# Optimization experiments

Hardware: AMD Instinct MI355X
Metric: run time of the kernel (lower is better)

Reference implementation:

```python
import jax, jax.numpy as jnp
import numpy as np

H = 512  # hidden_size


def setup_inputs() -> dict:
    key = jax.random.key(0)
    ks = jax.random.split(key, 8)
    B, L_tgt, L_src = 4, 32, 1024
    query = jax.random.normal(ks[0], (B, L_tgt, H), dtype=jnp.float32)
    states = jax.random.normal(ks[1], (B, L_src, 2 * H), dtype=jnp.float32)
    source_mask = jnp.ones((B, L_src), dtype=jnp.int32)
    s = 0.02
    Wq = jax.random.normal(ks[2], (H, 2 * H), dtype=jnp.float32) * s      # _linear_query.weight^T
    bq = jax.random.normal(ks[3], (2 * H,), dtype=jnp.float32) * s        # _linear_query.bias
    Ws = jax.random.normal(ks[4], (2 * H, 2 * H), dtype=jnp.float32) * s  # _linear_source.weight^T (no bias)
    v = jax.random.normal(ks[5], (2 * H,), dtype=jnp.float32) * s         # _v.weight (no bias)
    Wc = jax.random.normal(ks[6], (3 * H, H), dtype=jnp.float32) * s      # _context.weight^T
    bc = jax.random.normal(ks[7], (H,), dtype=jnp.float32) * s            # _context.bias
    return {"query": query, "states": states, "source_mask": source_mask,
            "Wq": Wq, "bq": bq, "Ws": Ws, "v": v, "Wc": Wc, "bc": bc}


def reference(query, states, source_mask, Wq, bq, Ws, v, Wc, bc):
    # Bahdanau additive attention.
    # query: (B, T, H), states: (B, S, 2H), source_mask: (B, S)
    qf = query @ Wq + bq                         # (B, T, 2H)
    sf = states @ Ws                             # (B, S, 2H)
    # alignments: v . tanh(qf[:, :, None] + sf[:, None, :])  -> (B, T, S)
    feats = jnp.tanh(qf[:, :, None, :] + sf[:, None, :, :])  # (B, T, S, 2H)
    alignments = jnp.einsum('btsd,d->bts', feats, v)
    # mask (B, S) -> (B, 1, S); masked positions get -inf before softmax
    alignments = jnp.where(source_mask[:, None, :].astype(bool), alignments, -jnp.inf)
    attentions = jax.nn.softmax(alignments, axis=2)           # (B, T, S)
    context = jnp.einsum('bts,bsd->btd', attentions, states)  # (B, T, 2H)
    concat_context = jnp.concatenate((context, query), axis=2)  # (B, T, 3H)
    attention_hidden = concat_context @ Wc + bc               # (B, T, H)
    attentions_t = jnp.swapaxes(attentions, 1, 2)             # (B, S, T)
    return (context, attention_hidden, attentions_t)
```

## Files before the change

### kernel.cpp

```cpp
#include <hip/hip_runtime.h>
#include <math.h>


typedef unsigned short u16;
typedef __bf16 bf16x8 __attribute__((ext_vector_type(8)));
typedef float floatx4 __attribute__((ext_vector_type(4)));

#define B_ 4
#define T_ 32
#define S_ 1024
#define H_ 512
#define D_ 1024
#define BT_ 128
#define TWO_LOG2E 2.8853900817779268f
#define LOG2E 1.4426950408889634f

__device__ __forceinline__ float bf2f(u16 u) {
  unsigned int i = ((unsigned int)u) << 16;
  return __builtin_bit_cast(float, i);
}
__device__ __forceinline__ u16 f2bf(float f) {
  unsigned int i = __builtin_bit_cast(unsigned int, f);
  i += 0x7fffu + ((i >> 16) & 1u);
  return (u16)(i >> 16);
}
__device__ __forceinline__ void ld_g2l_16(const u16* g, u16* l) {
  __builtin_amdgcn_global_load_lds((__attribute__((address_space(1))) void*)(u16*)g,
                                   (__attribute__((address_space(3))) void*)l, 16, 0, 0);
}


__global__ __launch_bounds__(256) void prep_fused5(const float* __restrict__ states, const float* __restrict__ Ws,
                                                   const float* __restrict__ query, const float* __restrict__ Wq,
                                                   const float* __restrict__ bq,
                                                   const float* __restrict__ Wc, const float* __restrict__ bc,
                                                   u16* __restrict__ sbf, u16* __restrict__ sbfT,
                                                   u16* __restrict__ WsT, float* __restrict__ qfp,
                                                   float* __restrict__ rowsum, float* __restrict__ hid) {
  __shared__ u16 tile[32][65];
  __shared__ float q[8][128];
  const int t = threadIdx.x;
  if (blockIdx.x < 512) {
    if (blockIdx.x == 0 && t < 128) rowsum[t] = 0.f;
    const int n0 = (blockIdx.x & 15) * 64, k0 = (blockIdx.x >> 4) * 32;
    const int kr = t >> 3, nc = (t & 7) * 8;
    const float* p = Ws + (size_t)(k0 + kr) * D_ + n0 + nc;
    float4 a = *(const float4*)p, b = *(const float4*)(p + 4);
    tile[kr][nc + 0] = f2bf(a.x); tile[kr][nc + 1] = f2bf(a.y);
    tile[kr][nc + 2] = f2bf(a.z); tile[kr][nc + 3] = f2bf(a.w);
    tile[kr][nc + 4] = f2bf(b.x); tile[kr][nc + 5] = f2bf(b.y);
    tile[kr][nc + 6] = f2bf(b.z); tile[kr][nc + 7] = f2bf(b.w);
    __syncthreads();
    const int nr = t >> 2, kc = (t & 3) * 8;
    union { uint4 v; u16 s[8]; } st;
#pragma unroll
    for (int i = 0; i < 8; ++i) st.s[i] = tile[kc + i][nr];
    *(uint4*)(WsT + (size_t)(n0 + nr) * D_ + k0 + kc) = st.v;
  } else if (blockIdx.x < 2560) {
    const int bid = blockIdx.x - 512;
    const int b = bid >> 9;
    const int r2 = bid & 511;
    const int d0 = (r2 & 15) * 64, s0 = (r2 >> 4) * 32;
    const int sr = t >> 3, dc = (t & 7) * 8;
    const float* p = states + ((size_t)b * S_ + s0 + sr) * D_ + d0 + dc;
    float4 a = *(const float4*)p, bb = *(const float4*)(p + 4);
    union { uint4 v; u16 s[8]; } pk;
    pk.s[0] = f2bf(a.x); pk.s[1] = f2bf(a.y); pk.s[2] = f2bf(a.z); pk.s[3] = f2bf(a.w);
    pk.s[4] = f2bf(bb.x); pk.s[5] = f2bf(bb.y); pk.s[6] = f2bf(bb.z); pk.s[7] = f2bf(bb.w);
    *(uint4*)(sbf + ((size_t)b * S_ + s0 + sr) * D_ + d0 + dc) = pk.v;
#pragma unroll
    for (int i = 0; i < 8; ++i) tile[sr][dc + i] = pk.s[i];
    __syncthreads();
    const int dr = t >> 2, sc = (t & 3) * 8;
    union { uint4 v; u16 s[8]; } st;
#pragma unroll
    for (int i = 0; i < 8; ++i) st.s[i] = tile[sc + i][dr];
    *(uint4*)(sbfT + ((size_t)b * D_ + d0 + dr) * S_ + s0 + sc) = st.v;
  } else if (blockIdx.x < 2816) {
    const int idx = blockIdx.x - 2560;
    const int c0 = (idx & 3) * 256, r0 = ((idx >> 2) & 15) * 8, ks = idx >> 6;
    const int k0 = ks * 128;
    for (int i = t; i < 8 * 128; i += 256) {
      const int rl = i >> 7, kk = i & 127;
      q[rl][kk] = query[(size_t)(r0 + rl) * H_ + k0 + kk];
    }
    __syncthreads();
    const int col = c0 + t;
    float acc[8] = {};
    for (int kk = 0; kk < 128; ++kk) {
      const float w = Wq[(size_t)(k0 + kk) * D_ + col];
#pragma unroll
      for (int r = 0; r < 8; ++r) acc[r] = fmaf(q[r][kk], w, acc[r]);
    }
    const float bb = (ks == 0) ? bq[col] : 0.f;
    float* dst = qfp + (size_t)ks * (BT_ * D_);
#pragma unroll
    for (int r = 0; r < 8; ++r)
      dst[(size_t)(r0 + r) * D_ + col] = TWO_LOG2E * (acc[r] + bb);
  } else {
    const int idx = blockIdx.x - 2816;
    const int c0 = (idx & 1) * 256, r0 = ((idx >> 1) & 15) * 8, ks = idx >> 5;
    const int k0 = ks * 128;
    for (int i = t; i < 8 * 128; i += 256) {
      const int rl = i >> 7, kk = i & 127;
      q[rl][kk] = query[(size_t)(r0 + rl) * H_ + k0 + kk];
    }
    __syncthreads();
    const int col = c0 + t;
    float acc[8] = {};
    for (int kk = 0; kk < 128; ++kk) {
      const float w = Wc[(size_t)(D_ + k0 + kk) * H_ + col];
#pragma unroll
      for (int r = 0; r < 8; ++r) acc[r] = fmaf(q[r][kk], w, acc[r]);
    }
    const float bb = (ks == 0) ? bc[col] : 0.f;
#pragma unroll
    for (int r = 0; r < 8; ++r)
      atomicAdd(&hid[(size_t)(r0 + r) * H_ + col], acc[r] + bb);
  }
}

__device__ __forceinline__ void f2f_stage(const u16* __restrict__ A, const u16* __restrict__ BT,
                                          u16* sAb, u16* sBb, int bm0, int bn0, int k0,
                                          int wv, int srow, int sp) {
#pragma unroll
  for (int j = 0; j < 4; ++j) {
    const int r = wv * 32 + j * 8 + srow;
    const int c = sp ^ (r & 7);
    ld_g2l_16(A + (size_t)(bm0 + r) * D_ + k0 + c * 8, sAb + (wv * 32 + j * 8) * 64);
  }
#pragma unroll
  for (int j = 0; j < 2; ++j) {
    const int r = wv * 16 + j * 8 + srow;
    const int c = sp ^ (r & 7);
    ld_g2l_16(BT + (size_t)(bn0 + r) * D_ + k0 + c * 8, sBb + (wv * 16 + j * 8) * 64);
  }
}

__device__ __forceinline__ void f2f_compute(const u16* sAb, const u16* sBb,
                                            int wm, int wn, int fm, int fq, floatx4 (&acc)[4][2]) {
#pragma unroll
  for (int win = 0; win < 2; ++win) {
    bf16x8 af[4], bfr[2];
#pragma unroll
    for (int i = 0; i < 4; ++i) {
      const int R = wm + i * 16 + fm;
      af[i] = *(const bf16x8*)&sAb[R * 64 + ((win * 4 + fq) ^ (R & 7)) * 8];
    }
#pragma unroll
    for (int j = 0; j < 2; ++j) {
      const int R = wn + j * 16 + fm;
      bfr[j] = *(const bf16x8*)&sBb[R * 64 + ((win * 4 + fq) ^ (R & 7)) * 8];
    }
#pragma unroll
    for (int i = 0; i < 4; ++i)
#pragma unroll
      for (int j = 0; j < 2; ++j)
        acc[i][j] = __builtin_amdgcn_mfma_f32_16x16x32_bf16(af[i], bfr[j], acc[i][j], 0, 0, 0);
  }
}

__global__ __launch_bounds__(256) void f2i_sfgemm(const u16* __restrict__ A, const u16* __restrict__ BT,
                                                  const float* __restrict__ qfp, float* __restrict__ Eq,
                                                  u16* __restrict__ Es) {
  __shared__ __align__(16) u16 sA[2][128 * 64];
  __shared__ __align__(16) u16 sB[2][64 * 64];
  const int bm0 = blockIdx.y * 128, bn0 = blockIdx.x * 64;
  const int t = threadIdx.x;
  const int wv = t >> 6, lane = t & 63;
  const int wm = (wv >> 1) * 64, wn = (wv & 1) * 32;
  const int fm = lane & 15, fq = lane >> 4;
  const int srow = lane >> 3, sp = lane & 7;

  {
    const int bid = blockIdx.y * 16 + blockIdx.x;
    const int idx = bid * 256 + t;
    const float s = qfp[idx] + qfp[BT_ * D_ + idx] +
                    qfp[2 * BT_ * D_ + idx] + qfp[3 * BT_ * D_ + idx];
    Eq[idx] = __builtin_amdgcn_exp2f(s);
  }

  floatx4 acc[4][2];
  const floatx4 fz = {0.f, 0.f, 0.f, 0.f};
#pragma unroll
  for (int i = 0; i < 4; ++i) { acc[i][0] = fz; acc[i][1] = fz; }

  f2f_stage(A, BT, sA[0], sB[0], bm0, bn0, 0, wv, srow, sp);
#pragma unroll 1
  for (int k0 = 0; k0 < D_; k0 += 128) {
    f2f_stage(A, BT, sA[1], sB[1], bm0, bn0, k0 + 64, wv, srow, sp);
    asm volatile("s_waitcnt vmcnt(6)" ::: "memory");
    __builtin_amdgcn_s_barrier();
    f2f_compute(sA[0], sB[0], wm, wn, fm, fq, acc);
    __builtin_amdgcn_s_barrier();
    if (k0 + 128 < D_) {
      f2f_stage(A, BT, sA[0], sB[0], bm0, bn0, k0 + 128, wv, srow, sp);
      asm volatile("s_waitcnt vmcnt(6)" ::: "memory");
    } else {
      asm volatile("s_waitcnt vmcnt(0)" ::: "memory");
    }
    __builtin_amdgcn_s_barrier();
    f2f_compute(sA[1], sB[1], wm, wn, fm, fq, acc);
    __builtin_amdgcn_s_barrier();
  }
#pragma unroll
  for (int i = 0; i < 4; ++i)
#pragma unroll
    for (int j = 0; j < 2; ++j)
#pragma unroll
      for (int r = 0; r < 4; ++r) {
        const int row = bm0 + wm + i * 16 + fq * 4 + r;
        const int col = bn0 + wn + j * 16 + fm;
        Es[(size_t)row * D_ + col] = f2bf(__builtin_amdgcn_exp2f(TWO_LOG2E * acc[i][j][r]));
      }
}

__global__ __launch_bounds__(256) void f3j_align(const float* __restrict__ Eq, const u16* __restrict__ Es,
                                                 const float* __restrict__ v, const int* __restrict__ mask,
                                                 u16* __restrict__ pbf, float* __restrict__ rowsum) {
  __shared__ float red[32][4];
  const int w = (blockIdx.x * 256 + threadIdx.x) >> 6;
  const int lane = threadIdx.x & 63;
  const int wv = threadIdx.x >> 6;
  const int b = w >> 9;
  const int s0 = (w & 511) * 2;
  const int msk0 = mask[(size_t)b * S_ + s0];
  const int msk1 = mask[(size_t)b * S_ + s0 + 1];
  float vm2[16], es0[16], es1[16];
  float sumv = 0.f;
  {
    union { uint4 u[2]; u16 h[16]; } ua, ub;
    const uint4* ep0 = (const uint4*)(Es + ((size_t)b * S_ + s0) * D_ + lane * 16);
    const uint4* ep1 = (const uint4*)(Es + ((size_t)b * S_ + s0 + 1) * D_ + lane * 16);
    ua.u[0] = ep0[0]; ua.u[1] = ep0[1];
    ub.u[0] = ep1[0]; ub.u[1] = ep1[1];
    const float4* vp = (const float4*)(v + lane * 16);
#pragma unroll
    for (int c = 0; c < 4; ++c) {
      const float4 w4 = vp[c];
      vm2[4 * c + 0] = -2.f * w4.x; vm2[4 * c + 1] = -2.f * w4.y;
      vm2[4 * c + 2] = -2.f * w4.z; vm2[4 * c + 3] = -2.f * w4.w;
      sumv += w4.x + w4.y + w4.z + w4.w;
    }
#pragma unroll
    for (int j = 0; j < 16; ++j) { es0[j] = bf2f(ua.h[j]); es1[j] = bf2f(ub.h[j]); }
  }
  const float* qbase = Eq + ((size_t)(b * T_)) * D_ + lane * 16;
  for (int tc = 0; tc < 8; ++tc) {
    float sa[4], sb[4];
#pragma unroll
    for (int ti = 0; ti < 4; ++ti) {
      const float4* qp = (const float4*)(qbase + (size_t)(tc * 4 + ti) * D_);
      float a0 = sumv, a1 = sumv;
#pragma unroll
      for (int c = 0; c < 4; ++c) {
        const float4 q4 = qp[c];
        const float xs[4] = {q4.x, q4.y, q4.z, q4.w};
#pragma unroll
        for (int u2 = 0; u2 < 4; ++u2) {
          const int j = 4 * c + u2;
          a0 = fmaf(vm2[j], __builtin_amdgcn_rcpf(fmaf(xs[u2], es0[j], 1.f)), a0);
          a1 = fmaf(vm2[j], __builtin_amdgcn_rcpf(fmaf(xs[u2], es1[j], 1.f)), a1);
        }
      }
      sa[ti] = a0; sb[ti] = a1;
    }
#pragma unroll
    for (int off = 32; off > 0; off >>= 1)
#pragma unroll
      for (int ti = 0; ti < 4; ++ti) {
        sa[ti] += __shfl_xor(sa[ti], off);
        sb[ti] += __shfl_xor(sb[ti], off);
      }
    if (lane == 0) {
#pragma unroll
      for (int ti = 0; ti < 4; ++ti) {
        const int tt = tc * 4 + ti;
        const float e0 = msk0 ? __builtin_amdgcn_exp2f(sa[ti] * LOG2E) : 0.f;
        const float e1 = msk1 ? __builtin_amdgcn_exp2f(sb[ti] * LOG2E) : 0.f;
        const u16 p0 = f2bf(e0), p1 = f2bf(e1);
        *(unsigned int*)&pbf[((size_t)(b * T_ + tt)) * S_ + s0] =
            (unsigned int)p0 | ((unsigned int)p1 << 16);
        red[tt][wv] = bf2f(p0) + bf2f(p1);
      }
    }
  }
  __syncthreads();
  if (threadIdx.x < 32) {
    const int bb = blockIdx.x >> 7;
    const float rs = red[threadIdx.x][0] + red[threadIdx.x][1] +
                     red[threadIdx.x][2] + red[threadIdx.x][3];
    atomicAdd(&rowsum[bb * 32 + threadIdx.x], rs);
  }
}

__global__ __launch_bounds__(256) void f5d_context(const u16* __restrict__ pbf, const u16* __restrict__ sbfT,
                                                   const float* __restrict__ rowsum,
                                                   float* __restrict__ ctx, float* __restrict__ out_at) {
  __shared__ float rinv[32];
  const int b = blockIdx.x >> 4, dt = blockIdx.x & 15;
  if (threadIdx.x < 32) rinv[threadIdx.x] = 1.f / rowsum[b * 32 + threadIdx.x];
  __syncthreads();
  const int wv = threadIdx.x >> 6, lane = threadIdx.x & 63;
  const int n0 = dt * 64 + wv * 16;
  const int fm = lane & 15, fq = lane >> 4;
  const floatx4 fz = {0.f, 0.f, 0.f, 0.f};
  floatx4 acc0 = fz, acc1 = fz;
  const u16* pa0 = pbf + ((size_t)b * T_ + fm) * S_ + fq * 8;
  const u16* pa1 = pbf + ((size_t)b * T_ + 16 + fm) * S_ + fq * 8;
  const u16* pb  = sbfT + ((size_t)b * D_ + n0 + fm) * S_ + fq * 8;
#pragma unroll 4
  for (int k0 = 0; k0 < S_; k0 += 32) {
    bf16x8 a0 = *(const bf16x8*)(pa0 + k0);
    bf16x8 a1 = *(const bf16x8*)(pa1 + k0);
    bf16x8 bb = *(const bf16x8*)(pb + k0);
    acc0 = __builtin_amdgcn_mfma_f32_16x16x32_bf16(a0, bb, acc0, 0, 0, 0);
    acc1 = __builtin_amdgcn_mfma_f32_16x16x32_bf16(a1, bb, acc1, 0, 0, 0);
  }
  const int col = n0 + fm;
#pragma unroll
  for (int r = 0; r < 4; ++r) {
    const int t0r = fq * 4 + r;
    ctx[((size_t)b * T_ + t0r) * D_ + col] = acc0[r] * rinv[t0r];
    ctx[((size_t)b * T_ + 16 + t0r) * D_ + col] = acc1[r] * rinv[16 + t0r];
  }
  const int s0 = dt * 64;
  for (int i = threadIdx.x; i < 64 * 32; i += 256) {
    const int tt = i >> 6, sl = i & 63;
    const float e = bf2f(pbf[((size_t)(b * T_ + tt)) * S_ + s0 + sl]);
    out_at[((size_t)(b * S_ + s0 + sl)) * T_ + tt] = e * rinv[tt];
  }
}

__global__ __launch_bounds__(256) void f6c_outproj(const float* __restrict__ ctx,
                                                   const float* __restrict__ Wc,
                                                   float* __restrict__ out_hid) {
  __shared__ float cq[16][128];
  const int c0 = blockIdx.x * 128, r0 = blockIdx.y * 16, k0 = blockIdx.z * 128;
  const int tid = threadIdx.x;
  const int cl = tid & 127, rh = tid >> 7;
  for (int i = tid; i < 16 * 128; i += 256) {
    const int rl = i >> 7, kk = i & 127;
    cq[rl][kk] = ctx[(size_t)(r0 + rl) * D_ + k0 + kk];
  }
  __syncthreads();
  float acc[8] = {};
  for (int kk = 0; kk < 128; ++kk) {
    const float w = Wc[(size_t)(k0 + kk) * H_ + c0 + cl];
#pragma unroll
    for (int rr = 0; rr < 8; ++rr) acc[rr] = fmaf(cq[rh * 8 + rr][kk], w, acc[rr]);
  }
#pragma unroll
  for (int rr = 0; rr < 8; ++rr)
    atomicAdd(&out_hid[(size_t)(r0 + rh * 8 + rr) * H_ + c0 + cl], acc[rr]);
}


__global__ __launch_bounds__(256) void prep_fused(const float* __restrict__ states, const float* __restrict__ Ws,
                                                  const float* __restrict__ query, const float* __restrict__ Wq,
                                                  const float* __restrict__ bq,
                                                  u16* __restrict__ sbf, u16* __restrict__ sbfT,
                                                  u16* __restrict__ WsT, float* __restrict__ qf) {
  __shared__ u16 tile[32][65];
  __shared__ float q[8][128];
  const int t = threadIdx.x;
  if (blockIdx.x < 512) {
    const int n0 = (blockIdx.x & 15) * 64, k0 = (blockIdx.x >> 4) * 32;
    const int kr = t >> 3, nc = (t & 7) * 8;
    const float* p = Ws + (size_t)(k0 + kr) * D_ + n0 + nc;
    float4 a = *(const float4*)p, b = *(const float4*)(p + 4);
    tile[kr][nc + 0] = f2bf(a.x); tile[kr][nc + 1] = f2bf(a.y);
    tile[kr][nc + 2] = f2bf(a.z); tile[kr][nc + 3] = f2bf(a.w);
    tile[kr][nc + 4] = f2bf(b.x); tile[kr][nc + 5] = f2bf(b.y);
    tile[kr][nc + 6] = f2bf(b.z); tile[kr][nc + 7] = f2bf(b.w);
    __syncthreads();
    const int nr = t >> 2, kc = (t & 3) * 8;
    union { uint4 v; u16 s[8]; } st;
#pragma unroll
    for (int i = 0; i < 8; ++i) st.s[i] = tile[kc + i][nr];
    *(uint4*)(WsT + (size_t)(n0 + nr) * D_ + k0 + kc) = st.v;
  } else if (blockIdx.x < 2560) {
    const int bid = blockIdx.x - 512;
    const int b = bid >> 9;
    const int r2 = bid & 511;
    const int d0 = (r2 & 15) * 64, s0 = (r2 >> 4) * 32;
    const int sr = t >> 3, dc = (t & 7) * 8;
    const float* p = states + ((size_t)b * S_ + s0 + sr) * D_ + d0 + dc;
    float4 a = *(const float4*)p, bb = *(const float4*)(p + 4);
    union { uint4 v; u16 s[8]; } pk;
    pk.s[0] = f2bf(a.x); pk.s[1] = f2bf(a.y); pk.s[2] = f2bf(a.z); pk.s[3] = f2bf(a.w);
    pk.s[4] = f2bf(bb.x); pk.s[5] = f2bf(bb.y); pk.s[6] = f2bf(bb.z); pk.s[7] = f2bf(bb.w);
    *(uint4*)(sbf + ((size_t)b * S_ + s0 + sr) * D_ + d0 + dc) = pk.v;
#pragma unroll
    for (int i = 0; i < 8; ++i) tile[sr][dc + i] = pk.s[i];
    __syncthreads();
    const int dr = t >> 2, sc = (t & 3) * 8;
    union { uint4 v; u16 s[8]; } st;
#pragma unroll
    for (int i = 0; i < 8; ++i) st.s[i] = tile[sc + i][dr];
    *(uint4*)(sbfT + ((size_t)b * D_ + d0 + dr) * S_ + s0 + sc) = st.v;
  } else {
    const int idx = blockIdx.x - 2560;
    const int c0 = (idx & 3) * 256, r0 = ((idx >> 2) & 15) * 8, k0 = (idx >> 6) * 128;
    for (int i = t; i < 8 * 128; i += 256) {
      const int rl = i >> 7, kk = i & 127;
      q[rl][kk] = query[(size_t)(r0 + rl) * H_ + k0 + kk];
    }
    __syncthreads();
    const int col = c0 + t;
    float acc[8] = {};
    for (int kk = 0; kk < 128; ++kk) {
      const float w = Wq[(size_t)(k0 + kk) * D_ + col];
#pragma unroll
      for (int r = 0; r < 8; ++r) acc[r] = fmaf(q[r][kk], w, acc[r]);
    }
    const float bb = (k0 == 0) ? bq[col] : 0.f;
#pragma unroll
    for (int r = 0; r < 8; ++r)
      atomicAdd(&qf[(size_t)(r0 + r) * D_ + col], TWO_LOG2E * (acc[r] + bb));
  }
}

__global__ __launch_bounds__(256) void f2e_sfgemm(const u16* __restrict__ A, const u16* __restrict__ BT,
                                                  u16* __restrict__ Cb) {
  __shared__ __align__(16) u16 sA[128 * 64];
  __shared__ __align__(16) u16 sB[64 * 64];
  const int bm0 = blockIdx.y * 128, bn0 = blockIdx.x * 64;
  const int t = threadIdx.x;
  const int wv = t >> 6, lane = t & 63;
  const int wm = (wv >> 1) * 64, wn = (wv & 1) * 32;
  const int fm = lane & 15, fq = lane >> 4;
  const int srow = lane >> 3, sp = lane & 7;

  floatx4 acc[4][2];
  const floatx4 fz = {0.f, 0.f, 0.f, 0.f};
#pragma unroll
  for (int i = 0; i < 4; ++i) { acc[i][0] = fz; acc[i][1] = fz; }

  for (int k0 = 0; k0 < D_; k0 += 64) {
    __syncthreads();
#pragma unroll
    for (int j = 0; j < 4; ++j) {
      const int r = wv * 32 + j * 8 + srow;
      const int c = sp ^ (r & 7);
      ld_g2l_16(A + (size_t)(bm0 + r) * D_ + k0 + c * 8, &sA[(wv * 32 + j * 8) * 64]);
    }
#pragma unroll
    for (int j = 0; j < 2; ++j) {
      const int r = wv * 16 + j * 8 + srow;
      const int c = sp ^ (r & 7);
      ld_g2l_16(BT + (size_t)(bn0 + r) * D_ + k0 + c * 8, &sB[(wv * 16 + j * 8) * 64]);
    }
    __syncthreads();
#pragma unroll
    for (int win = 0; win < 2; ++win) {
      bf16x8 af[4], bfr[2];
#pragma unroll
      for (int i = 0; i < 4; ++i) {
        const int R = wm + i * 16 + fm;
        af[i] = *(const bf16x8*)&sA[R * 64 + ((win * 4 + fq) ^ (R & 7)) * 8];
      }
#pragma unroll
      for (int j = 0; j < 2; ++j) {
        const int R = wn + j * 16 + fm;
        bfr[j] = *(const bf16x8*)&sB[R * 64 + ((win * 4 + fq) ^ (R & 7)) * 8];
      }
#pragma unroll
      for (int i = 0; i < 4; ++i)
#pragma unroll
        for (int j = 0; j < 2; ++j)
          acc[i][j] = __builtin_amdgcn_mfma_f32_16x16x32_bf16(af[i], bfr[j], acc[i][j], 0, 0, 0);
    }
  }
#pragma unroll
  for (int i = 0; i < 4; ++i)
#pragma unroll
    for (int j = 0; j < 2; ++j)
#pragma unroll
      for (int r = 0; r < 4; ++r) {
        const int row = bm0 + wm + i * 16 + fq * 4 + r;
        const int col = bn0 + wn + j * 16 + fm;
        Cb[(size_t)row * D_ + col] = f2bf(TWO_LOG2E * acc[i][j][r]);
      }
}

__global__ __launch_bounds__(256, 6) void f3f_align(const float* __restrict__ qf, const u16* __restrict__ sfb,
                                                    const float* __restrict__ v, float* __restrict__ alg) {
  const int wid = (blockIdx.x * 256 + threadIdx.x) >> 6;
  const int lane = threadIdx.x & 63;
  const int b = wid >> 10, s = wid & 1023;
  const int t0 = blockIdx.y * 16;
  float vr[16], sr[16];
  {
    union { uint4 v[2]; u16 s[16]; } u;
    const uint4* sp = (const uint4*)(sfb + (size_t)wid * D_ + lane * 16);
    u.v[0] = sp[0]; u.v[1] = sp[1];
    const float* vp = v + lane * 16;
#pragma unroll
    for (int c = 0; c < 4; ++c) {
      float4 w = *(const float4*)(vp + 4 * c);
      vr[4 * c + 0] = w.x; vr[4 * c + 1] = w.y; vr[4 * c + 2] = w.z; vr[4 * c + 3] = w.w;
    }
#pragma unroll
    for (int j = 0; j < 16; ++j) sr[j] = bf2f(u.s[j]);
  }
  float sum[16];
#pragma unroll
  for (int tt = 0; tt < 16; ++tt) sum[tt] = 0.f;

  const float* qbase = qf + ((size_t)(b * T_ + t0)) * D_ + lane * 16;
  for (int tt = 0; tt < 16; ++tt) {
    const float4* qp = (const float4*)(qbase + (size_t)tt * D_);
    float acc = 0.f;
#pragma unroll
    for (int c = 0; c < 4; ++c) {
      float4 q4 = qp[c];
      float xs[4] = {q4.x, q4.y, q4.z, q4.w};
#pragma unroll
      for (int u2 = 0; u2 < 4; ++u2) {
        const int j = 4 * c + u2;
        const float x = xs[u2] + sr[j];
        const float e = __builtin_amdgcn_exp2f(x);
        acc = fmaf(vr[j], fmaf(-2.f, __builtin_amdgcn_rcpf(e + 1.f), 1.f), acc);
      }
    }
    sum[tt] = acc;
  }
#pragma unroll
  for (int off = 32; off > 0; off >>= 1)
#pragma unroll
    for (int tt = 0; tt < 16; ++tt) sum[tt] += __shfl_xor(sum[tt], off);
  if (lane == 0) {
#pragma unroll
    for (int tt = 0; tt < 16; ++tt)
      alg[((size_t)(b * T_ + t0 + tt)) * S_ + s] = sum[tt];
  }
}

__global__ __launch_bounds__(256) void f4b_softmax(const float* __restrict__ alg, const int* __restrict__ mask,
                                                   float* __restrict__ out_at, u16* __restrict__ pbf) {
  const int r = blockIdx.x;
  const int b = r >> 5, t = r & 31;
  const int tid = threadIdx.x;
  __shared__ float red[256];
  float a[4];
#pragma unroll
  for (int jj = 0; jj < 4; ++jj) {
    const int s = tid + 256 * jj;
    const float x = alg[(size_t)r * S_ + s];
    a[jj] = (mask[(size_t)b * S_ + s] != 0) ? x : -3.0e38f;
  }
  float m = fmaxf(fmaxf(a[0], a[1]), fmaxf(a[2], a[3]));
  red[tid] = m; __syncthreads();
  for (int st = 128; st > 0; st >>= 1) { if (tid < st) red[tid] = fmaxf(red[tid], red[tid + st]); __syncthreads(); }
  m = red[0]; __syncthreads();
  float e[4], lsum = 0.f;
#pragma unroll
  for (int jj = 0; jj < 4; ++jj) {
    e[jj] = (a[jj] > -1.0e38f) ? expf(a[jj] - m) : 0.f;
    lsum += e[jj];
  }
  red[tid] = lsum; __syncthreads();
  for (int st = 128; st > 0; st >>= 1) { if (tid < st) red[tid] += red[tid + st]; __syncthreads(); }
  const float rs = 1.f / red[0];
#pragma unroll
  for (int jj = 0; jj < 4; ++jj) {
    const int s = tid + 256 * jj;
    const float p = e[jj] * rs;
    out_at[((size_t)b * S_ + s) * T_ + t] = p;
    pbf[(size_t)r * S_ + s] = f2bf(p);
  }
}

__global__ __launch_bounds__(256) void f5c_context(const u16* __restrict__ pbf, const u16* __restrict__ sbfT,
                                                   float* __restrict__ ctx) {
  const int b = blockIdx.x >> 4, dt = blockIdx.x & 15;
  const int wv = threadIdx.x >> 6, lane = threadIdx.x & 63;
  const int n0 = dt * 64 + wv * 16;
  const int fm = lane & 15, fq = lane >> 4;
  const floatx4 fz = {0.f, 0.f, 0.f, 0.f};
  floatx4 acc0 = fz, acc1 = fz;
  const u16* pa0 = pbf + ((size_t)b * T_ + fm) * S_ + fq * 8;
  const u16* pa1 = pbf + ((size_t)b * T_ + 16 + fm) * S_ + fq * 8;
  const u16* pb  = sbfT + ((size_t)b * D_ + n0 + fm) * S_ + fq * 8;
#pragma unroll 4
  for (int k0 = 0; k0 < S_; k0 += 32) {
    bf16x8 a0 = *(const bf16x8*)(pa0 + k0);
    bf16x8 a1 = *(const bf16x8*)(pa1 + k0);
    bf16x8 bb = *(const bf16x8*)(pb + k0);
    acc0 = __builtin_amdgcn_mfma_f32_16x16x32_bf16(a0, bb, acc0, 0, 0, 0);
    acc1 = __builtin_amdgcn_mfma_f32_16x16x32_bf16(a1, bb, acc1, 0, 0, 0);
  }
  const int col = n0 + fm;
#pragma unroll
  for (int r = 0; r < 4; ++r) {
    ctx[((size_t)b * T_ + fq * 4 + r) * D_ + col] = acc0[r];
    ctx[((size_t)b * T_ + 16 + fq * 4 + r) * D_ + col] = acc1[r];
  }
}

__global__ __launch_bounds__(256) void f6b_outproj(const float* __restrict__ ctx, const float* __restrict__ query,
                                                   const float* __restrict__ Wc, const float* __restrict__ bc,
                                                   float* __restrict__ out_hid) {
  __shared__ float cq[16][128];
  const int c0 = blockIdx.x * 128, r0 = blockIdx.y * 16, k0 = blockIdx.z * 128;
  const int tid = threadIdx.x;
  const int cl = tid & 127, rh = tid >> 7;
  for (int i = tid; i < 16 * 128; i += 256) {
    const int rl = i >> 7, kk = i & 127;
    const int k = k0 + kk, row = r0 + rl;
    cq[rl][kk] = (k < D_) ? ctx[(size_t)row * D_ + k] : query[(size_t)row * H_ + k - D_];
  }
  __syncthreads();
  float acc[8] = {};
  for (int kk = 0; kk < 128; ++kk) {
    const float w = Wc[(size_t)(k0 + kk) * H_ + c0 + cl];
#pragma unroll
    for (int rr = 0; rr < 8; ++rr) acc[rr] = fmaf(cq[rh * 8 + rr][kk], w, acc[rr]);
  }
  const float bb = (blockIdx.z == 0) ? bc[c0 + cl] : 0.f;
#pragma unroll
  for (int rr = 0; rr < 8; ++rr)
    atomicAdd(&out_hid[(size_t)(r0 + rh * 8 + rr) * H_ + c0 + cl], acc[rr] + bb);
}


__global__ __launch_bounds__(256) void kc_cvt(const float* __restrict__ in, u16* __restrict__ out) {
  const size_t i0 = ((size_t)blockIdx.x * 256 + threadIdx.x) * 8;
  float4 a = *(const float4*)(in + i0);
  float4 b = *(const float4*)(in + i0 + 4);
  union { uint4 v; u16 s[8]; } r;
  r.s[0] = f2bf(a.x); r.s[1] = f2bf(a.y); r.s[2] = f2bf(a.z); r.s[3] = f2bf(a.w);
  r.s[4] = f2bf(b.x); r.s[5] = f2bf(b.y); r.s[6] = f2bf(b.z); r.s[7] = f2bf(b.w);
// ... 128 lines not shown
    *(uint4*)&sA[arow * 40 + akc + 8] = pa.v[1];
    *(uint4*)&sB[brow * 40 + bkc] = vb;
    __syncthreads();
    bf16x8 af[4], bfr[2];
#pragma unroll
    for (int i = 0; i < 4; ++i) af[i] = *(const bf16x8*)&sA[(wm + i * 16 + fm) * 40 + fq * 8];
#pragma unroll
    for (int j = 0; j < 2; ++j) bfr[j] = *(const bf16x8*)&sB[(wn + j * 16 + fm) * 40 + fq * 8];
#pragma unroll
    for (int i = 0; i < 4; ++i)
#pragma unroll
      for (int j = 0; j < 2; ++j)
        acc[i][j] = __builtin_amdgcn_mfma_f32_16x16x32_bf16(af[i], bfr[j], acc[i][j], 0, 0, 0);
  }
#pragma unroll
  for (int i = 0; i < 4; ++i)
#pragma unroll
    for (int j = 0; j < 2; ++j)
#pragma unroll
      for (int r = 0; r < 4; ++r) {
        const int row = bm0 + wm + i * 16 + fq * 4 + r;
        const int col = bn0 + wn + j * 16 + fm;
        Cb[(size_t)row * D_ + col] = f2bf(TWO_LOG2E * acc[i][j][r]);
      }
}

__global__ __launch_bounds__(256) void f4_softmax(const float* __restrict__ alg, const int* __restrict__ mask,
                                                  float* __restrict__ attn) {
  const int r = blockIdx.x;
  const int b = r >> 5;
  const int tid = threadIdx.x;
  __shared__ float red[256];
  float a[4];
#pragma unroll
  for (int jj = 0; jj < 4; ++jj) {
    const int s = tid + 256 * jj;
    const float x = alg[(size_t)r * S_ + s];
    a[jj] = (mask[(size_t)b * S_ + s] != 0) ? x : -3.0e38f;
  }
  float m = fmaxf(fmaxf(a[0], a[1]), fmaxf(a[2], a[3]));
  red[tid] = m; __syncthreads();
  for (int st = 128; st > 0; st >>= 1) { if (tid < st) red[tid] = fmaxf(red[tid], red[tid + st]); __syncthreads(); }
  m = red[0]; __syncthreads();
  float e[4], lsum = 0.f;
#pragma unroll
  for (int jj = 0; jj < 4; ++jj) {
    e[jj] = (a[jj] > -1.0e38f) ? expf(a[jj] - m) : 0.f;
    lsum += e[jj];
  }
  red[tid] = lsum; __syncthreads();
  for (int st = 128; st > 0; st >>= 1) { if (tid < st) red[tid] += red[tid + st]; __syncthreads(); }
  const float rs = 1.f / red[0];
#pragma unroll
  for (int jj = 0; jj < 4; ++jj)
    attn[(size_t)r * S_ + tid + 256 * jj] = e[jj] * rs;
}

__global__ __launch_bounds__(256) void f5b_context(const float* __restrict__ attn, const u16* __restrict__ sbf,
                                                   float* __restrict__ ctx, float* __restrict__ out_at) {
  __shared__ float at[16][64];
  const int s0 = blockIdx.x * 64, t0 = blockIdx.y * 16, b = blockIdx.z;
  const int tid = threadIdx.x;
  for (int i = tid; i < 16 * 64; i += 256) {
    const int tl = i >> 6, sl = i & 63;
    at[tl][sl] = attn[(size_t)(b * T_ + t0 + tl) * S_ + s0 + sl];
  }
  __syncthreads();
  for (int i = tid; i < 64 * 16; i += 256) {
    const int sl = i >> 4, tl = i & 15;
    out_at[((size_t)b * S_ + s0 + sl) * T_ + t0 + tl] = at[tl][sl];
  }
  float acc[16][4] = {};
  for (int sl = 0; sl < 64; ++sl) {
    const u16* srow = sbf + ((size_t)b * S_ + s0 + sl) * D_ + tid;
    float sv[4];
#pragma unroll
    for (int jj = 0; jj < 4; ++jj) sv[jj] = bf2f(srow[256 * jj]);
#pragma unroll
    for (int tl = 0; tl < 16; ++tl) {
      const float w = at[tl][sl];
#pragma unroll
      for (int jj = 0; jj < 4; ++jj) acc[tl][jj] = fmaf(w, sv[jj], acc[tl][jj]);
    }
  }
#pragma unroll
  for (int tl = 0; tl < 16; ++tl)
#pragma unroll
    for (int jj = 0; jj < 4; ++jj)
      atomicAdd(&ctx[(size_t)(b * T_ + t0 + tl) * D_ + tid + 256 * jj], acc[tl][jj]);
}

__global__ __launch_bounds__(256) void f5_context(const float* __restrict__ attn, const float* __restrict__ states,
                                                  float* __restrict__ ctx, float* __restrict__ out_at) {
  __shared__ float at[16][64];
  const int s0 = blockIdx.x * 64, t0 = blockIdx.y * 16, b = blockIdx.z;
  const int tid = threadIdx.x;
  for (int i = tid; i < 16 * 64; i += 256) {
    const int tl = i >> 6, sl = i & 63;
    at[tl][sl] = attn[(size_t)(b * T_ + t0 + tl) * S_ + s0 + sl];
  }
  __syncthreads();
  for (int i = tid; i < 64 * 16; i += 256) {
    const int sl = i >> 4, tl = i & 15;
    out_at[((size_t)b * S_ + s0 + sl) * T_ + t0 + tl] = at[tl][sl];
  }
  float acc[16][4] = {};
  for (int sl = 0; sl < 64; ++sl) {
    const float* srow = states + ((size_t)b * S_ + s0 + sl) * D_ + tid;
    float sv[4];
#pragma unroll
    for (int jj = 0; jj < 4; ++jj) sv[jj] = srow[256 * jj];
#pragma unroll
    for (int tl = 0; tl < 16; ++tl) {
      const float w = at[tl][sl];
#pragma unroll
      for (int jj = 0; jj < 4; ++jj) acc[tl][jj] = fmaf(w, sv[jj], acc[tl][jj]);
    }
  }
#pragma unroll
  for (int tl = 0; tl < 16; ++tl)
#pragma unroll
    for (int jj = 0; jj < 4; ++jj)
      atomicAdd(&ctx[(size_t)(b * T_ + t0 + tl) * D_ + tid + 256 * jj], acc[tl][jj]);
}


__global__ __launch_bounds__(256) void k1_qf(const float* __restrict__ query, const float* __restrict__ Wq,
                                             const float* __restrict__ bq, float* __restrict__ qf) {
  const int r = blockIdx.x;
  const int tid = threadIdx.x;
  __shared__ float q[H_];
  for (int i = tid; i < H_; i += 256) q[i] = query[(size_t)r * H_ + i];
  __syncthreads();
#pragma unroll
  for (int jj = 0; jj < 4; ++jj) {
    const int j = tid + 256 * jj;
    float acc = bq[j];
    for (int k = 0; k < H_; ++k) acc = fmaf(q[k], Wq[(size_t)k * D_ + j], acc);
    qf[(size_t)r * D_ + j] = acc;
  }
}

__global__ __launch_bounds__(256) void k23_align(const float* __restrict__ states, const float* __restrict__ Ws,
                                                 const float* __restrict__ v, const float* __restrict__ qf,
                                                 float* __restrict__ alg) {
  const int b = blockIdx.x >> 6;
  const int s0 = (blockIdx.x & 63) * 16;
  const int tid = threadIdx.x, lane = tid & 63, wv = tid >> 6;
  __shared__ u16 stL[16 * D_];
  __shared__ float vvL[D_];
  __shared__ float red[16 * 4];
  for (int i = tid; i < 16 * D_; i += 256) {
    const int row = i >> 10, col = i & (D_ - 1);
    stL[i] = f2bf(states[((size_t)b * S_ + s0 + row) * D_ + col]);
  }
  for (int i = tid; i < D_; i += 256) vvL[i] = v[i];
  __syncthreads();
  float acc[64];
#pragma unroll
  for (int i = 0; i < 64; ++i) acc[i] = 0.f;
#pragma unroll 4
  for (int k = 0; k < D_; ++k) {
    float wsv[4];
#pragma unroll
    for (int jj = 0; jj < 4; ++jj) wsv[jj] = Ws[(size_t)k * D_ + tid + 256 * jj];
#pragma unroll
    for (int i = 0; i < 16; ++i) {
      const float sv = bf2f(stL[i * D_ + k]);
#pragma unroll
      for (int jj = 0; jj < 4; ++jj) acc[i * 4 + jj] = fmaf(sv, wsv[jj], acc[i * 4 + jj]);
    }
  }
  for (int t = 0; t < T_; ++t) {
    float qv[4];
#pragma unroll
    for (int jj = 0; jj < 4; ++jj) qv[jj] = qf[((size_t)b * T_ + t) * D_ + tid + 256 * jj];
    float part[16];
#pragma unroll
    for (int i = 0; i < 16; ++i) {
      float p = 0.f;
#pragma unroll
      for (int jj = 0; jj < 4; ++jj)
        p = fmaf(vvL[tid + 256 * jj], tanhf(qv[jj] + acc[i * 4 + jj]), p);
      part[i] = p;
    }
#pragma unroll
    for (int i = 0; i < 16; ++i) {
      float x = part[i];
#pragma unroll
      for (int off = 32; off > 0; off >>= 1) x += __shfl_xor(x, off);
      if (lane == 0) red[i * 4 + wv] = x;
    }
    __syncthreads();
    if (tid < 16)
      alg[((size_t)b * T_ + t) * S_ + s0 + tid] =
          red[tid * 4 + 0] + red[tid * 4 + 1] + red[tid * 4 + 2] + red[tid * 4 + 3];
    __syncthreads();
  }
}

__global__ __launch_bounds__(256) void k4_softmax(const float* __restrict__ alg, const int* __restrict__ mask,
                                                  float* __restrict__ attn) {
  const int r = blockIdx.x;
  const int b = r >> 5;
  const int tid = threadIdx.x;
  __shared__ float red[256];
  float a[4];
#pragma unroll
  for (int jj = 0; jj < 4; ++jj) {
    const int s = tid + 256 * jj;
    const float x = alg[(size_t)r * S_ + s];
    a[jj] = (mask[(size_t)b * S_ + s] != 0) ? x : -3.0e38f;
  }
  float m = fmaxf(fmaxf(a[0], a[1]), fmaxf(a[2], a[3]));
  red[tid] = m; __syncthreads();
  for (int st = 128; st > 0; st >>= 1) { if (tid < st) red[tid] = fmaxf(red[tid], red[tid + st]); __syncthreads(); }
  m = red[0]; __syncthreads();
  float e[4], lsum = 0.f;
#pragma unroll
  for (int jj = 0; jj < 4; ++jj) {
    e[jj] = (a[jj] > -1.0e38f) ? expf(a[jj] - m) : 0.f;
    lsum += e[jj];
  }
  red[tid] = lsum; __syncthreads();
  for (int st = 128; st > 0; st >>= 1) { if (tid < st) red[tid] += red[tid + st]; __syncthreads(); }
  const float rs = 1.f / red[0];
#pragma unroll
  for (int jj = 0; jj < 4; ++jj)
    attn[(size_t)r * S_ + tid + 256 * jj] = e[jj] * rs;
}

__global__ __launch_bounds__(256) void k56_ctx_proj(const float* __restrict__ attn, const float* __restrict__ states,
                                                    const float* __restrict__ query, const float* __restrict__ Wc,
                                                    const float* __restrict__ bc,
                                                    float* __restrict__ out_ctx, float* __restrict__ out_hid,
                                                    float* __restrict__ out_at) {
  const int r = blockIdx.x;
  const int b = r >> 5, t = r & (T_ - 1);
  const int tid = threadIdx.x;
  __shared__ float pr[S_];
  __shared__ float cq[D_ + H_];
  for (int s = tid; s < S_; s += 256) pr[s] = attn[(size_t)r * S_ + s];
  __syncthreads();
  for (int s = tid; s < S_; s += 256) out_at[((size_t)b * S_ + s) * T_ + t] = pr[s];
  float acc[4] = {0.f, 0.f, 0.f, 0.f};
  for (int s = 0; s < S_; ++s) {
    const float w = pr[s];
    const float* srow = states + ((size_t)b * S_ + s) * D_ + tid;
#pragma unroll
    for (int jj = 0; jj < 4; ++jj) acc[jj] = fmaf(w, srow[256 * jj], acc[jj]);
  }
#pragma unroll
  for (int jj = 0; jj < 4; ++jj) {
    cq[tid + 256 * jj] = acc[jj];
    out_ctx[(size_t)r * D_ + tid + 256 * jj] = acc[jj];
  }
  for (int i = tid; i < H_; i += 256) cq[D_ + i] = query[(size_t)r * H_ + i];
  __syncthreads();
#pragma unroll
  for (int jj = 0; jj < 2; ++jj) {
    const int n = tid + 256 * jj;
    float h = bc[n];
    for (int k = 0; k < D_ + H_; ++k) h = fmaf(cq[k], Wc[(size_t)k * H_ + n], h);
    out_hid[(size_t)r * H_ + n] = h;
  }
}

extern "C" void kernel_launch(void* const* d_in, const int* in_sizes, int n_in,
                              void* d_out, int out_size, void* d_ws, size_t ws_size,
                              hipStream_t stream) {
  const float* query  = (const float*)d_in[0];
  const float* states = (const float*)d_in[1];
  const int*   mask   = (const int*)d_in[2];
  const float* Wq     = (const float*)d_in[3];
  const float* bq     = (const float*)d_in[4];
  const float* Ws     = (const float*)d_in[5];
  const float* v      = (const float*)d_in[6];
  const float* Wc     = (const float*)d_in[7];
  const float* bc     = (const float*)d_in[8];

  float* A  = (float*)d_out;
  float* Bh = A + (size_t)BT_ * D_;
  float* C  = Bh + (size_t)BT_ * H_;

  char* ws = (char*)d_ws;
  u16*   sfb  = (u16*)(ws + 0);
  u16*   WsT  = (u16*)(ws + 8388608);
  float* alg  = (float*)(ws + 10485760);
  u16*   sbf  = (u16*)(ws + 11010048);
  u16*   sbfT = (u16*)(ws + 19398656);
  u16*   pbf  = (u16*)(ws + 27787264);

  const size_t WS_T1 = 11010048;
  const size_t WS_T2 = 19398656;
  const size_t WS_T3 = 28049408;
  const size_t WS_T4 = 36962816;

  if (ws_size >= WS_T4) {
    float* qfp  = (float*)(ws + 0);
    u16*   Es16 = (u16*)(ws + 28049408);
    float* Eq4  = (float*)(ws + 36438016);
    float* rsum = (float*)(ws + 36962304);
    (void)hipMemsetAsync(Bh, 0, (size_t)BT_ * H_ * 4, stream);
    prep_fused5<<<2944, 256, 0, stream>>>(states, Ws, query, Wq, bq, Wc, bc,
                                          sbf, sbfT, WsT, qfp, rsum, Bh);
    f2i_sfgemm<<<dim3(16, 32), 256, 0, stream>>>(sbf, WsT, qfp, Eq4, Es16);
    f3j_align<<<512, 256, 0, stream>>>(Eq4, Es16, v, mask, pbf, rsum);
    f5d_context<<<64, 256, 0, stream>>>(pbf, sbfT, rsum, A, C);
    f6c_outproj<<<dim3(4, 8, 8), 256, 0, stream>>>(A, Wc, Bh);
  } else if (ws_size >= WS_T3) {
    (void)hipMemsetAsync(A, 0, (size_t)(BT_ * D_ + BT_ * H_) * 4, stream);
    prep_fused<<<2816, 256, 0, stream>>>(states, Ws, query, Wq, bq, sbf, sbfT, WsT, A);
    f2e_sfgemm<<<dim3(16, 32), 256, 0, stream>>>(sbf, WsT, sfb);
    f3f_align<<<dim3(1024, 2), 256, 0, stream>>>(A, sfb, v, alg);
    f4b_softmax<<<BT_, 256, 0, stream>>>(alg, mask, C, pbf);
    f5c_context<<<64, 256, 0, stream>>>(pbf, sbfT, A);
    f6b_outproj<<<dim3(4, 8, 12), 256, 0, stream>>>(A, query, Wc, bc, Bh);
  } else if (ws_size >= WS_T1) {
    float* attn = alg;
    (void)hipMemsetAsync(A, 0, (size_t)(BT_ * D_ + BT_ * H_) * 4, stream);
    f1b_qf<<<dim3(4, 16, 4), 256, 0, stream>>>(query, Wq, bq, A);
    f0_transpose<<<dim3(16, 32), 256, 0, stream>>>(Ws, WsT);
    const int tier2 = (ws_size >= WS_T2);
    if (tier2) {
      kc_cvt<<<2048, 256, 0, stream>>>(states, sbf);
      f2c_sfgemm<<<dim3(16, 32), 256, 0, stream>>>(sbf, WsT, sfb);
    } else {
      f2d_sfgemm<<<dim3(16, 32), 256, 0, stream>>>(states, WsT, sfb);
    }
    f3f_align<<<dim3(1024, 2), 256, 0, stream>>>(A, sfb, v, C);
    (void)hipMemsetAsync(A, 0, (size_t)BT_ * D_ * 4, stream);
    f4_softmax<<<BT_, 256, 0, stream>>>(C, mask, attn);
    if (tier2)
      f5b_context<<<dim3(16, 2, 4), 256, 0, stream>>>(attn, sbf, A, C);
    else
      f5_context<<<dim3(16, 2, 4), 256, 0, stream>>>(attn, states, A, C);
    f6b_outproj<<<dim3(4, 8, 12), 256, 0, stream>>>(A, query, Wc, bc, Bh);
  } else {
    k1_qf<<<BT_, 256, 0, stream>>>(query, Wq, bq, A);
    k23_align<<<B_ * (S_ / 16), 256, 0, stream>>>(states, Ws, v, A, C);
    k4_softmax<<<BT_, 256, 0, stream>>>(C, mask, A);
    k56_ctx_proj<<<BT_, 256, 0, stream>>>(A, states, query, Wc, bc, A, Bh, C);
  }
}
```

Measured before the change: 171.9 us.

## Reorder prep blocks, widen align per-wave work, split context over S with reduction

The prep kernel now schedules the long-running query GEMV blocks (Wq and Wc) first, ahead of the many short transpose and convert blocks, to cut the tail. The align kernel has each wave handle four source positions instead of two, so each query load is reused more and half as many blocks are launched. The context kernel goes from 64 to 256 blocks: each block's four waves split the S reduction and combine their partial results through shared memory, giving more parallelism for the small MFMA GEMM. The costs are extra LDS traffic and a barrier in the context kernel, plus higher register pressure in align.

Result: faster. 165.3 us, median of 2 (-3.9%).

```diff
diff --git a/kernel.cpp b/kernel.cpp
--- a/kernel.cpp
+++ b/kernel.cpp
@@ -30,7 +30,7 @@
 }
 
 
-__global__ __launch_bounds__(256) void prep_fused5(const float* __restrict__ states, const float* __restrict__ Ws,
+__global__ __launch_bounds__(256) void prep_fused6(const float* __restrict__ states, const float* __restrict__ Ws,
                                                    const float* __restrict__ query, const float* __restrict__ Wq,
                                                    const float* __restrict__ bq,
                                                    const float* __restrict__ Wc, const float* __restrict__ bc,
@@ -40,9 +40,51 @@
   __shared__ u16 tile[32][65];
   __shared__ float q[8][128];
   const int t = threadIdx.x;
-  if (blockIdx.x < 512) {
-    if (blockIdx.x == 0 && t < 128) rowsum[t] = 0.f;
-    const int n0 = (blockIdx.x & 15) * 64, k0 = (blockIdx.x >> 4) * 32;
+  if (blockIdx.x < 256) {
+    const int idx = blockIdx.x;
+    const int c0 = (idx & 3) * 256, r0 = ((idx >> 2) & 15) * 8, ks = idx >> 6;
+    const int k0 = ks * 128;
+    for (int i = t; i < 8 * 128; i += 256) {
+      const int rl = i >> 7, kk = i & 127;
+      q[rl][kk] = query[(size_t)(r0 + rl) * H_ + k0 + kk];
+    }
+    __syncthreads();
+    const int col = c0 + t;
+    float acc[8] = {};
+    for (int kk = 0; kk < 128; ++kk) {
+      const float w = Wq[(size_t)(k0 + kk) * D_ + col];
+#pragma unroll
+      for (int r = 0; r < 8; ++r) acc[r] = fmaf(q[r][kk], w, acc[r]);
+    }
+    const float bb = (ks == 0) ? bq[col] : 0.f;
+    float* dst = qfp + (size_t)ks * (BT_ * D_);
+#pragma unroll
+    for (int r = 0; r < 8; ++r)
+      dst[(size_t)(r0 + r) * D_ + col] = TWO_LOG2E * (acc[r] + bb);
+  } else if (blockIdx.x < 384) {
+    const int idx = blockIdx.x - 256;
+    const int c0 = (idx & 1) * 256, r0 = ((idx >> 1) & 15) * 8, ks = idx >> 5;
+    const int k0 = ks * 128;
+    for (int i = t; i < 8 * 128; i += 256) {
+      const int rl = i >> 7, kk = i & 127;
+      q[rl][kk] = query[(size_t)(r0 + rl) * H_ + k0 + kk];
+    }
+    __syncthreads();
+    const int col = c0 + t;
+    float acc[8] = {};
+    for (int kk = 0; kk < 128; ++kk) {
+      const float w = Wc[(size_t)(D_ + k0 + kk) * H_ + col];
+#pragma unroll
+      for (int r = 0; r < 8; ++r) acc[r] = fmaf(q[r][kk], w, acc[r]);
+    }
+    const float bb = (ks == 0) ? bc[col] : 0.f;
+#pragma unroll
+    for (int r = 0; r < 8; ++r)
+      atomicAdd(&hid[(size_t)(r0 + r) * H_ + col], acc[r] + bb);
+  } else if (blockIdx.x < 896) {
+    const int bid = blockIdx.x - 384;
+    if (bid == 0 && t < 128) rowsum[t] = 0.f;
+    const int n0 = (bid & 15) * 64, k0 = (bid >> 4) * 32;
     const int kr = t >> 3, nc = (t & 7) * 8;
     const float* p = Ws + (size_t)(k0 + kr) * D_ + n0 + nc;
     float4 a = *(const float4*)p, b = *(const float4*)(p + 4);
@@ -56,8 +98,8 @@
 #pragma unroll
     for (int i = 0; i < 8; ++i) st.s[i] = tile[kc + i][nr];
     *(uint4*)(WsT + (size_t)(n0 + nr) * D_ + k0 + kc) = st.v;
-  } else if (blockIdx.x < 2560) {
-    const int bid = blockIdx.x - 512;
+  } else {
+    const int bid = blockIdx.x - 896;
     const int b = bid >> 9;
     const int r2 = bid & 511;
     const int d0 = (r2 & 15) * 64, s0 = (r2 >> 4) * 32;
@@ -76,47 +118,6 @@
 #pragma unroll
     for (int i = 0; i < 8; ++i) st.s[i] = tile[sc + i][dr];
     *(uint4*)(sbfT + ((size_t)b * D_ + d0 + dr) * S_ + s0 + sc) = st.v;
-  } else if (blockIdx.x < 2816) {
-    const int idx = blockIdx.x - 2560;
-    const int c0 = (idx & 3) * 256, r0 = ((idx >> 2) & 15) * 8, ks = idx >> 6;
-    const int k0 = ks * 128;
-    for (int i = t; i < 8 * 128; i += 256) {
-      const int rl = i >> 7, kk = i & 127;
-      q[rl][kk] = query[(size_t)(r0 + rl) * H_ + k0 + kk];
-    }
-    __syncthreads();
-    const int col = c0 + t;
-    float acc[8] = {};
-    for (int kk = 0; kk < 128; ++kk) {
-      const float w = Wq[(size_t)(k0 + kk) * D_ + col];
-#pragma unroll
-      for (int r = 0; r < 8; ++r) acc[r] = fmaf(q[r][kk], w, acc[r]);
-    }
-    const float bb = (ks == 0) ? bq[col] : 0.f;
-    float* dst = qfp + (size_t)ks * (BT_ * D_);
-#pragma unroll
-    for (int r = 0; r < 8; ++r)
-      dst[(size_t)(r0 + r) * D_ + col] = TWO_LOG2E * (acc[r] + bb);
-  } else {
-    const int idx = blockIdx.x - 2816;
-    const int c0 = (idx & 1) * 256, r0 = ((idx >> 1) & 15) * 8, ks = idx >> 5;
-    const int k0 = ks * 128;
-    for (int i = t; i < 8 * 128; i += 256) {
-      const int rl = i >> 7, kk = i & 127;
-      q[rl][kk] = query[(size_t)(r0 + rl) * H_ + k0 + kk];
-    }
-    __syncthreads();
-    const int col = c0 + t;
-    float acc[8] = {};
-    for (int kk = 0; kk < 128; ++kk) {
-      const float w = Wc[(size_t)(D_ + k0 + kk) * H_ + col];
-#pragma unroll
-      for (int r = 0; r < 8; ++r) acc[r] = fmaf(q[r][kk], w, acc[r]);
-    }
-    const float bb = (ks == 0) ? bc[col] : 0.f;
-#pragma unroll
-    for (int r = 0; r < 8; ++r)
-      atomicAdd(&hid[(size_t)(r0 + r) * H_ + col], acc[r] + bb);
   }
 }
 
@@ -215,25 +216,30 @@
       }
 }
 
-__global__ __launch_bounds__(256) void f3j_align(const float* __restrict__ Eq, const u16* __restrict__ Es,
+__global__ __launch_bounds__(256) void f3k_align(const float* __restrict__ Eq, const u16* __restrict__ Es,
                                                  const float* __restrict__ v, const int* __restrict__ mask,
                                                  u16* __restrict__ pbf, float* __restrict__ rowsum) {
   __shared__ float red[32][4];
-  const int w = (blockIdx.x * 256 + threadIdx.x) >> 6;
-  const int lane = threadIdx.x & 63;
-  const int wv = threadIdx.x >> 6;
-  const int b = w >> 9;
-  const int s0 = (w & 511) * 2;
-  const int msk0 = mask[(size_t)b * S_ + s0];
-  const int msk1 = mask[(size_t)b * S_ + s0 + 1];
-  float vm2[16], es0[16], es1[16];
+  const int wv = threadIdx.x >> 6, lane = threadIdx.x & 63;
+  const int w = blockIdx.x * 4 + wv;
+  const int b = w >> 8;
+  const int s0 = (w & 255) * 4;
+  const int m0 = mask[(size_t)b * S_ + s0 + 0];
+  const int m1 = mask[(size_t)b * S_ + s0 + 1];
+  const int m2 = mask[(size_t)b * S_ + s0 + 2];
+  const int m3 = mask[(size_t)b * S_ + s0 + 3];
+  float vm2[16], es0[16], es1[16], es2[16], es3[16];
   float sumv = 0.f;
   {
-    union { uint4 u[2]; u16 h[16]; } ua, ub;
-    const uint4* ep0 = (const uint4*)(Es + ((size_t)b * S_ + s0) * D_ + lane * 16);
+    union { uint4 u[2]; u16 h[16]; } u0, u1, u2, u3;
+    const uint4* ep0 = (const uint4*)(Es + ((size_t)b * S_ + s0 + 0) * D_ + lane * 16);
     const uint4* ep1 = (const uint4*)(Es + ((size_t)b * S_ + s0 + 1) * D_ + lane * 16);
-    ua.u[0] = ep0[0]; ua.u[1] = ep0[1];
-    ub.u[0] = ep1[0]; ub.u[1] = ep1[1];
+    const uint4* ep2 = (const uint4*)(Es + ((size_t)b * S_ + s0 + 2) * D_ + lane * 16);
+    const uint4* ep3 = (const uint4*)(Es + ((size_t)b * S_ + s0 + 3) * D_ + lane * 16);
+    u0.u[0] = ep0[0]; u0.u[1] = ep0[1];
+    u1.u[0] = ep1[0]; u1.u[1] = ep1[1];
+    u2.u[0] = ep2[0]; u2.u[1] = ep2[1];
+    u3.u[0] = ep3[0]; u3.u[1] = ep3[1];
     const float4* vp = (const float4*)(v + lane * 16);
 #pragma unroll
     for (int c = 0; c < 4; ++c) {
@@ -243,15 +249,18 @@
       sumv += w4.x + w4.y + w4.z + w4.w;
     }
 #pragma unroll
-    for (int j = 0; j < 16; ++j) { es0[j] = bf2f(ua.h[j]); es1[j] = bf2f(ub.h[j]); }
+    for (int j = 0; j < 16; ++j) {
+      es0[j] = bf2f(u0.h[j]); es1[j] = bf2f(u1.h[j]);
+      es2[j] = bf2f(u2.h[j]); es3[j] = bf2f(u3.h[j]);
+    }
   }
   const float* qbase = Eq + ((size_t)(b * T_)) * D_ + lane * 16;
   for (int tc = 0; tc < 8; ++tc) {
-    float sa[4], sb[4];
+    float sa[4], sb[4], sc[4], sd[4];
 #pragma unroll
     for (int ti = 0; ti < 4; ++ti) {
       const float4* qp = (const float4*)(qbase + (size_t)(tc * 4 + ti) * D_);
-      float a0 = sumv, a1 = sumv;
+      float a0 = sumv, a1 = sumv, a2 = sumv, a3 = sumv;
 #pragma unroll
       for (int c = 0; c < 4; ++c) {
         const float4 q4 = qp[c];
@@ -261,9 +270,11 @@
           const int j = 4 * c + u2;
           a0 = fmaf(vm2[j], __builtin_amdgcn_rcpf(fmaf(xs[u2], es0[j], 1.f)), a0);
           a1 = fmaf(vm2[j], __builtin_amdgcn_rcpf(fmaf(xs[u2], es1[j], 1.f)), a1);
+          a2 = fmaf(vm2[j], __builtin_amdgcn_rcpf(fmaf(xs[u2], es2[j], 1.f)), a2);
+          a3 = fmaf(vm2[j], __builtin_amdgcn_rcpf(fmaf(xs[u2], es3[j], 1.f)), a3);
         }
       }
-      sa[ti] = a0; sb[ti] = a1;
+      sa[ti] = a0; sb[ti] = a1; sc[ti] = a2; sd[ti] = a3;
     }
 #pragma unroll
     for (int off = 32; off > 0; off >>= 1)
@@ -271,64 +282,80 @@
       for (int ti = 0; ti < 4; ++ti) {
         sa[ti] += __shfl_xor(sa[ti], off);
         sb[ti] += __shfl_xor(sb[ti], off);
+        sc[ti] += __shfl_xor(sc[ti], off);
+        sd[ti] += __shfl_xor(sd[ti], off);
       }
     if (lane == 0) {
 #pragma unroll
       for (int ti = 0; ti < 4; ++ti) {
         const int tt = tc * 4 + ti;
-        const float e0 = msk0 ? __builtin_amdgcn_exp2f(sa[ti] * LOG2E) : 0.f;
-        const float e1 = msk1 ? __builtin_amdgcn_exp2f(sb[ti] * LOG2E) : 0.f;
-        const u16 p0 = f2bf(e0), p1 = f2bf(e1);
-        *(unsigned int*)&pbf[((size_t)(b * T_ + tt)) * S_ + s0] =
-            (unsigned int)p0 | ((unsigned int)p1 << 16);
-        red[tt][wv] = bf2f(p0) + bf2f(p1);
+        const float e0 = m0 ? __builtin_amdgcn_exp2f(sa[ti] * LOG2E) : 0.f;
+        const float e1 = m1 ? __builtin_amdgcn_exp2f(sb[ti] * LOG2E) : 0.f;
+        const float e2 = m2 ? __builtin_amdgcn_exp2f(sc[ti] * LOG2E) : 0.f;
+        const float e3 = m3 ? __builtin_amdgcn_exp2f(sd[ti] * LOG2E) : 0.f;
+        const u16 p0 = f2bf(e0), p1 = f2bf(e1), p2 = f2bf(e2), p3 = f2bf(e3);
+        uint2 pk;
+        pk.x = (unsigned int)p0 | ((unsigned int)p1 << 16);
+        pk.y = (unsigned int)p2 | ((unsigned int)p3 << 16);
+        *(uint2*)&pbf[((size_t)(b * T_ + tt)) * S_ + s0] = pk;
+        red[tt][wv] = bf2f(p0) + bf2f(p1) + bf2f(p2) + bf2f(p3);
       }
     }
   }
   __syncthreads();
   if (threadIdx.x < 32) {
-    const int bb = blockIdx.x >> 7;
+    const int bb = blockIdx.x >> 6;
     const float rs = red[threadIdx.x][0] + red[threadIdx.x][1] +
                      red[threadIdx.x][2] + red[threadIdx.x][3];
     atomicAdd(&rowsum[bb * 32 + threadIdx.x], rs);
   }
 }
 
-__global__ __launch_bounds__(256) void f5d_context(const u16* __restrict__ pbf, const u16* __restrict__ sbfT,
+__global__ __launch_bounds__(256) void f5e_context(const u16* __restrict__ pbf, const u16* __restrict__ sbfT,
                                                    const float* __restrict__ rowsum,
                                                    float* __restrict__ ctx, float* __restrict__ out_at) {
   __shared__ float rinv[32];
-  const int b = blockIdx.x >> 4, dt = blockIdx.x & 15;
+  __shared__ float red[4][64][9];
+  const int b = blockIdx.x >> 6, dt = blockIdx.x & 63;
+  const int wv = threadIdx.x >> 6, lane = threadIdx.x & 63;
   if (threadIdx.x < 32) rinv[threadIdx.x] = 1.f / rowsum[b * 32 + threadIdx.x];
-  __syncthreads();
-  const int wv = threadIdx.x >> 6, lane = threadIdx.x & 63;
-  const int n0 = dt * 64 + wv * 16;
+  const int n0 = dt * 16;
   const int fm = lane & 15, fq = lane >> 4;
   const floatx4 fz = {0.f, 0.f, 0.f, 0.f};
   floatx4 acc0 = fz, acc1 = fz;
-  const u16* pa0 = pbf + ((size_t)b * T_ + fm) * S_ + fq * 8;
-  const u16* pa1 = pbf + ((size_t)b * T_ + 16 + fm) * S_ + fq * 8;
-  const u16* pb  = sbfT + ((size_t)b * D_ + n0 + fm) * S_ + fq * 8;
-#pragma unroll 4
-  for (int k0 = 0; k0 < S_; k0 += 32) {
+  const u16* pa0 = pbf + ((size_t)b * T_ + fm) * S_ + wv * 256 + fq * 8;
+  const u16* pa1 = pa0 + (size_t)16 * S_;
+  const u16* pb  = sbfT + ((size_t)b * D_ + n0 + fm) * S_ + wv * 256 + fq * 8;
+#pragma unroll
+  for (int k0 = 0; k0 < 256; k0 += 32) {
     bf16x8 a0 = *(const bf16x8*)(pa0 + k0);
     bf16x8 a1 = *(const bf16x8*)(pa1 + k0);
     bf16x8 bb = *(const bf16x8*)(pb + k0);
     acc0 = __builtin_amdgcn_mfma_f32_16x16x32_bf16(a0, bb, acc0, 0, 0, 0);
     acc1 = __builtin_amdgcn_mfma_f32_16x16x32_bf16(a1, bb, acc1, 0, 0, 0);
   }
-  const int col = n0 + fm;
 #pragma unroll
   for (int r = 0; r < 4; ++r) {
-    const int t0r = fq * 4 + r;
-    ctx[((size_t)b * T_ + t0r) * D_ + col] = acc0[r] * rinv[t0r];
-    ctx[((size_t)b * T_ + 16 + t0r) * D_ + col] = acc1[r] * rinv[16 + t0r];
-  }
-  const int s0 = dt * 64;
-  for (int i = threadIdx.x; i < 64 * 32; i += 256) {
-    const int tt = i >> 6, sl = i & 63;
-    const float e = bf2f(pbf[((size_t)(b * T_ + tt)) * S_ + s0 + sl]);
-    out_at[((size_t)(b * S_ + s0 + sl)) * T_ + tt] = e * rinv[tt];
+    red[wv][lane][r] = acc0[r];
+    red[wv][lane][4 + r] = acc1[r];
+  }
+  __syncthreads();
+  const int s0a = dt * 16;
+  for (int i = threadIdx.x; i < 512; i += 256) {
+    const int tt = i & 31, sl = i >> 5;
+    const float e = bf2f(pbf[((size_t)(b * T_ + tt)) * S_ + s0a + sl]);
+    out_at[((size_t)(b * S_ + s0a + sl)) * T_ + tt] = e * rinv[tt];
+  }
+  if (wv == 0) {
+#pragma unroll
+    for (int r = 0; r < 4; ++r) {
+      const float v0 = red[0][lane][r] + red[1][lane][r] + red[2][lane][r] + red[3][lane][r];
+      const float v1 = red[0][lane][4 + r] + red[1][lane][4 + r] +
+                       red[2][lane][4 + r] + red[3][lane][4 + r];
+      const int t0r = fq * 4 + r;
+      ctx[((size_t)b * T_ + t0r) * D_ + n0 + fm] = v0 * rinv[t0r];
+      ctx[((size_t)b * T_ + 16 + t0r) * D_ + n0 + fm] = v1 * rinv[16 + t0r];
+    }
   }
 }
 
@@ -1063,11 +1090,11 @@
     float* Eq4  = (float*)(ws + 36438016);
     float* rsum = (float*)(ws + 36962304);
     (void)hipMemsetAsync(Bh, 0, (size_t)BT_ * H_ * 4, stream);
-    prep_fused5<<<2944, 256, 0, stream>>>(states, Ws, query, Wq, bq, Wc, bc,
+    prep_fused6<<<2944, 256, 0, stream>>>(states, Ws, query, Wq, bq, Wc, bc,
                                           sbf, sbfT, WsT, qfp, rsum, Bh);
     f2i_sfgemm<<<dim3(16, 32), 256, 0, stream>>>(sbf, WsT, qfp, Eq4, Es16);
-    f3j_align<<<512, 256, 0, stream>>>(Eq4, Es16, v, mask, pbf, rsum);
-    f5d_context<<<64, 256, 0, stream>>>(pbf, sbfT, rsum, A, C);
+    f3k_align<<<256, 256, 0, stream>>>(Eq4, Es16, v, mask, pbf, rsum);
+    f5e_context<<<256, 256, 0, stream>>>(pbf, sbfT, rsum, A, C);
     f6c_outproj<<<dim3(4, 8, 8), 256, 0, stream>>>(A, Wc, Bh);
   } else if (ws_size >= WS_T3) {
     (void)hipMemsetAsync(A, 0, (size_t)(BT_ * D_ + BT_ * H_) * 4, stream);
```
